# Optimization experiments

Hardware: AMD Instinct MI355X
Metric: run time of the kernel (lower is better)

## Reference

```python
import jax, jax.numpy as jnp
import numpy as np

N_NODES = 50000
N_EDGES = 600000
IN_CH = 64
HID = 128
N_GRAPHS = 64
EPS = 0.0  # GINEConv default eps


def setup_inputs() -> dict:
    key = jax.random.key(0)
    ks = jax.random.split(key, 16)
    x = jax.random.normal(ks[0], (N_NODES, IN_CH), dtype=jnp.float32)
    edge_index = jax.random.randint(ks[1], (2, N_EDGES), 0, N_NODES, dtype=jnp.int64)
    edge_attr = jax.random.normal(ks[2], (N_EDGES, 3), dtype=jnp.float32)
    batch = jnp.sort(jax.random.randint(ks[3], (N_NODES,), 0, N_GRAPHS, dtype=jnp.int64))
    s = lambda fan_in: 1.0 / np.sqrt(fan_in)
    # conv1: edge lin (3->IN_CH), mlp (IN_CH->HID->HID)
    el1_w = jax.random.uniform(ks[4], (3, IN_CH), minval=-s(3), maxval=s(3))
    el1_b = jnp.zeros((IN_CH,), jnp.float32)
    w1a = jax.random.uniform(ks[5], (IN_CH, HID), minval=-s(IN_CH), maxval=s(IN_CH))
    b1a = jnp.zeros((HID,), jnp.float32)
    w1b = jax.random.uniform(ks[6], (HID, HID), minval=-s(HID), maxval=s(HID))
    b1b = jnp.zeros((HID,), jnp.float32)
    # conv2: edge lin (3->HID), mlp (HID->HID->HID)
    el2_w = jax.random.uniform(ks[7], (3, HID), minval=-s(3), maxval=s(3))
    el2_b = jnp.zeros((HID,), jnp.float32)
    w2a = jax.random.uniform(ks[8], (HID, HID), minval=-s(HID), maxval=s(HID))
    b2a = jnp.zeros((HID,), jnp.float32)
    w2b = jax.random.uniform(ks[9], (HID, HID), minval=-s(HID), maxval=s(HID))
    b2b = jnp.zeros((HID,), jnp.float32)
    return dict(x=x, edge_index=edge_index, edge_attr=edge_attr, batch=batch,
                el1_w=el1_w, el1_b=el1_b, w1a=w1a, b1a=b1a, w1b=w1b, b1b=b1b,
                el2_w=el2_w, el2_b=el2_b, w2a=w2a, b2a=b2a, w2b=w2b, b2b=b2b)


def _gine_conv(x, src, dst, edge_attr, el_w, el_b, wa, ba, wb, bb):
    # message: relu(x_j + Lin(edge_attr)), aggregated (sum) at target nodes
    e = edge_attr @ el_w + el_b              # [E, d]
    msg = jax.nn.relu(x[src] + e)            # [E, d]
    agg = jax.ops.segment_sum(msg, dst, num_segments=x.shape[0])  # [N, d]
    h = (1.0 + EPS) * x + agg
    h = jax.nn.relu(h @ wa + ba) @ wb + bb   # MLP
    return h


def reference(x, edge_index, edge_attr, batch,
              el1_w, el1_b, w1a, b1a, w1b, b1b,
              el2_w, el2_b, w2a, b2a, w2b, b2b):
    src, dst = edge_index[0], edge_index[1]
    h = jax.nn.relu(_gine_conv(x, src, dst, edge_attr, el1_w, el1_b, w1a, b1a, w1b, b1b))
    h = jax.nn.relu(_gine_conv(h, src, dst, edge_attr, el2_w, el2_b, w2a, b2a, w2b, b2b))
    # global mean pool per graph
    sums = jax.ops.segment_sum(h, batch, num_segments=N_GRAPHS)
    cnt = jax.ops.segment_sum(jnp.ones((h.shape[0],), h.dtype), batch, num_segments=N_GRAPHS)
    return sums / jnp.maximum(cnt, 1.0)[:, None]
```

## Files before the change

kernel.cpp:

```cpp
#include <hip/hip_runtime.h>

#define N_NODES 50000
#define N_EDGES 600000
#define N_PAD 50048
#define IN_CH 64
#define HID 128
#define N_GRAPHS 64
#define CAP 64
#define CAP_SHIFT 6

typedef __attribute__((ext_vector_type(8))) short bf16x8;
typedef __attribute__((ext_vector_type(4))) float f32x4;

__device__ __forceinline__ float bf2f(unsigned short u) {
    union { unsigned int i; float f; } v; v.i = ((unsigned int)u) << 16; return v.f;
}
__device__ __forceinline__ unsigned short f2bf(float f) {
    union { float f; unsigned int i; } v; v.f = f;
    unsigned int u = v.i;
    return (unsigned short)((u + 0x7FFFu + ((u >> 16) & 1u)) >> 16);
}


__global__ void prep_kernel(const float* __restrict__ x,
                            const float* __restrict__ w1a, const float* __restrict__ w1b,
                            const float* __restrict__ w2a, const float* __restrict__ w2b,
                            const int* __restrict__ batch,
                            unsigned short* __restrict__ xbf,
                            unsigned short* __restrict__ waT1, unsigned short* __restrict__ wbT1,
                            unsigned short* __restrict__ waT2, unsigned short* __restrict__ wbT2,
                            int* __restrict__ deg, float* __restrict__ out,
                            float* __restrict__ inv_cnt) {
    int i = blockIdx.x * blockDim.x + threadIdx.x;
    if (i < N_NODES * IN_CH) xbf[i] = f2bf(x[i]);
    if (i < N_NODES) deg[i] = 0;
    if (i < N_GRAPHS * HID) out[i] = 0.f;
    if (i < N_GRAPHS) {
        int g = i;
        int lo = 0, hi = N_NODES;
        while (lo < hi) { int mid = (lo + hi) >> 1; if (batch[mid] < g) lo = mid + 1; else hi = mid; }
        int start = lo;
        lo = 0; hi = N_NODES;
        while (lo < hi) { int mid = (lo + hi) >> 1; if (batch[mid] <= g) lo = mid + 1; else hi = mid; }
        float c = (float)(lo - start);
        inv_cnt[g] = 1.0f / (c > 1.0f ? c : 1.0f);
    }
    if (i < IN_CH * HID) {
        int k = i / HID, n = i % HID;
        waT1[n * IN_CH + k] = f2bf(w1a[i]);
    }
    if (i < HID * HID) {
        int k = i / HID, n = i % HID;
        wbT1[n * HID + k] = f2bf(w1b[i]);
        waT2[n * HID + k] = f2bf(w2a[i]);
        wbT2[n * HID + k] = f2bf(w2b[i]);
    }
}

__global__ void build_kernel(const int* __restrict__ ei,
                             const float* __restrict__ ea,
                             int* __restrict__ deg,
                             uint2* __restrict__ edata) {
    int i = blockIdx.x * blockDim.x + threadIdx.x;
    if (i >= N_EDGES) return;
    int s = ei[i];
    int d = ei[N_EDGES + i];
    float a0 = ea[3 * (size_t)i], a1 = ea[3 * (size_t)i + 1], a2 = ea[3 * (size_t)i + 2];
    int p = atomicAdd(&deg[d], 1);
    if (p < CAP)
        edata[((size_t)d << CAP_SHIFT) + p] =
            make_uint2((unsigned)s | ((unsigned)f2bf(a0) << 16),
                       (unsigned)f2bf(a1) | ((unsigned)f2bf(a2) << 16));
}

__global__ void gather64_kernel(const unsigned short* __restrict__ xin,
                                const uint2* __restrict__ edata,
                                const int* __restrict__ deg,
                                const float* __restrict__ elw,
                                const float* __restrict__ elb,
                                unsigned short* __restrict__ sg) {
    constexpr int K = IN_CH;
    constexpr int NPB = 4;
    const int node0 = blockIdx.x * NPB;
    const int t = threadIdx.x;
    const int c = t & 63, half = t >> 6;
    const float w0 = elw[c], w1 = elw[K + c], w2 = elw[2 * K + c], eb = elb[c];

    auto term = [&](uint2 e, unsigned short row) -> float {
        float ev = bf2f((unsigned short)(e.x >> 16)) * w0 +
                   bf2f((unsigned short)(e.y & 0xFFFF)) * w1 +
                   bf2f((unsigned short)(e.y >> 16)) * w2 + eb;
        float m = bf2f(row) + ev;
        return m > 0.f ? m : 0.f;
    };

    for (int i = 0; i < NPB; i += 2) {
        int node = node0 + i + half;
        float acc = bf2f(xin[(size_t)node * K + c]);
        int dn = deg[node]; if (dn > CAP) dn = CAP;
        int jb = node << CAP_SHIFT, je = jb + dn;
        int j = jb;
        for (; j + 8 <= je; j += 8) {
            uint2 e0 = edata[j],     e1 = edata[j + 1], e2 = edata[j + 2], e3 = edata[j + 3];
            uint2 e4 = edata[j + 4], e5 = edata[j + 5], e6 = edata[j + 6], e7 = edata[j + 7];
            unsigned short r0 = xin[(size_t)(e0.x & 0xFFFF) * K + c];
            unsigned short r1 = xin[(size_t)(e1.x & 0xFFFF) * K + c];
            unsigned short r2 = xin[(size_t)(e2.x & 0xFFFF) * K + c];
            unsigned short r3 = xin[(size_t)(e3.x & 0xFFFF) * K + c];
            unsigned short r4 = xin[(size_t)(e4.x & 0xFFFF) * K + c];
            unsigned short r5 = xin[(size_t)(e5.x & 0xFFFF) * K + c];
            unsigned short r6 = xin[(size_t)(e6.x & 0xFFFF) * K + c];
            unsigned short r7 = xin[(size_t)(e7.x & 0xFFFF) * K + c];
            acc += term(e0, r0) + term(e1, r1) + term(e2, r2) + term(e3, r3)
                 + term(e4, r4) + term(e5, r5) + term(e6, r6) + term(e7, r7);
        }
        for (; j + 4 <= je; j += 4) {
            uint2 e0 = edata[j], e1 = edata[j + 1], e2 = edata[j + 2], e3 = edata[j + 3];
            unsigned short r0 = xin[(size_t)(e0.x & 0xFFFF) * K + c];
            unsigned short r1 = xin[(size_t)(e1.x & 0xFFFF) * K + c];
            unsigned short r2 = xin[(size_t)(e2.x & 0xFFFF) * K + c];
            unsigned short r3 = xin[(size_t)(e3.x & 0xFFFF) * K + c];
            acc += term(e0, r0) + term(e1, r1) + term(e2, r2) + term(e3, r3);
        }
        for (; j < je; j++) {
            uint2 e0 = edata[j];
            acc += term(e0, xin[(size_t)(e0.x & 0xFFFF) * K + c]);
        }
        sg[(size_t)node * K + c] = f2bf(acc);
    }
}

__global__ void gather128_kernel(const unsigned short* __restrict__ xin,
                                 const uint2* __restrict__ edata,
                                 const int* __restrict__ deg,
                                 const float* __restrict__ elw,
                                 const float* __restrict__ elb,
                                 unsigned short* __restrict__ sg) {
    const int t = threadIdx.x;
    const int w = t >> 6, l = t & 63;
    const unsigned* x32 = (const unsigned*)xin;
    unsigned* sg32 = (unsigned*)sg;
    const int c0 = 2 * l;
    const float w00 = elw[c0],           w01 = elw[c0 + 1];
    const float w10 = elw[HID + c0],     w11 = elw[HID + c0 + 1];
    const float w20 = elw[2 * HID + c0], w21 = elw[2 * HID + c0 + 1];
    const float eb0 = elb[c0],           eb1 = elb[c0 + 1];
    const int nA = (blockIdx.x * 4 + w) * 2;
    const int nB = nA + 1;

    unsigned svA = x32[(size_t)nA * 64 + l];
    unsigned svB = x32[(size_t)nB * 64 + l];
    float a0 = bf2f((unsigned short)(svA & 0xFFFF));
    float a1 = bf2f((unsigned short)(svA >> 16));
    float b0 = bf2f((unsigned short)(svB & 0xFFFF));
    float b1 = bf2f((unsigned short)(svB >> 16));

    auto term2 = [&](uint2 e, unsigned r, float& p0, float& p1) {
        float A0 = bf2f((unsigned short)(e.x >> 16));
        float A1 = bf2f((unsigned short)(e.y & 0xFFFF));
        float A2 = bf2f((unsigned short)(e.y >> 16));
        float ev0 = A0 * w00 + A1 * w10 + A2 * w20 + eb0;
        float ev1 = A0 * w01 + A1 * w11 + A2 * w21 + eb1;
        float m0 = bf2f((unsigned short)(r & 0xFFFF)) + ev0;
        float m1 = bf2f((unsigned short)(r >> 16)) + ev1;
        p0 += m0 > 0.f ? m0 : 0.f;
        p1 += m1 > 0.f ? m1 : 0.f;
    };

    int dA = deg[nA]; if (dA > CAP) dA = CAP;
    int dB = deg[nB]; if (dB > CAP) dB = CAP;
    int ja = nA << CAP_SHIFT; const int jaE = ja + dA;
    int jb = nB << CAP_SHIFT; const int jbE = jb + dB;
    while (ja + 4 <= jaE && jb + 4 <= jbE) {
        uint2 eA0 = edata[ja],     eA1 = edata[ja + 1], eA2 = edata[ja + 2], eA3 = edata[ja + 3];
        uint2 eB0 = edata[jb],     eB1 = edata[jb + 1], eB2 = edata[jb + 2], eB3 = edata[jb + 3];
        unsigned rA0 = x32[(size_t)(eA0.x & 0xFFFF) * 64 + l];
        unsigned rA1 = x32[(size_t)(eA1.x & 0xFFFF) * 64 + l];
        unsigned rA2 = x32[(size_t)(eA2.x & 0xFFFF) * 64 + l];
        unsigned rA3 = x32[(size_t)(eA3.x & 0xFFFF) * 64 + l];
        unsigned rB0 = x32[(size_t)(eB0.x & 0xFFFF) * 64 + l];
        unsigned rB1 = x32[(size_t)(eB1.x & 0xFFFF) * 64 + l];
        unsigned rB2 = x32[(size_t)(eB2.x & 0xFFFF) * 64 + l];
        unsigned rB3 = x32[(size_t)(eB3.x & 0xFFFF) * 64 + l];
        term2(eA0, rA0, a0, a1); term2(eA1, rA1, a0, a1);
        term2(eA2, rA2, a0, a1); term2(eA3, rA3, a0, a1);
        term2(eB0, rB0, b0, b1); term2(eB1, rB1, b0, b1);
        term2(eB2, rB2, b0, b1); term2(eB3, rB3, b0, b1);
        ja += 4; jb += 4;
    }
    for (; ja + 4 <= jaE; ja += 4) {
        uint2 e0 = edata[ja], e1 = edata[ja + 1], e2 = edata[ja + 2], e3 = edata[ja + 3];
        unsigned r0 = x32[(size_t)(e0.x & 0xFFFF) * 64 + l];
        unsigned r1 = x32[(size_t)(e1.x & 0xFFFF) * 64 + l];
        unsigned r2 = x32[(size_t)(e2.x & 0xFFFF) * 64 + l];
        unsigned r3 = x32[(size_t)(e3.x & 0xFFFF) * 64 + l];
        term2(e0, r0, a0, a1); term2(e1, r1, a0, a1);
        term2(e2, r2, a0, a1); term2(e3, r3, a0, a1);
    }
    for (; ja < jaE; ja++) {
        uint2 e0 = edata[ja];
        term2(e0, x32[(size_t)(e0.x & 0xFFFF) * 64 + l], a0, a1);
    }
    for (; jb + 4 <= jbE; jb += 4) {
        uint2 e0 = edata[jb], e1 = edata[jb + 1], e2 = edata[jb + 2], e3 = edata[jb + 3];
        unsigned r0 = x32[(size_t)(e0.x & 0xFFFF) * 64 + l];
        unsigned r1 = x32[(size_t)(e1.x & 0xFFFF) * 64 + l];
        unsigned r2 = x32[(size_t)(e2.x & 0xFFFF) * 64 + l];
        unsigned r3 = x32[(size_t)(e3.x & 0xFFFF) * 64 + l];
        term2(e0, r0, b0, b1); term2(e1, r1, b0, b1);
        term2(e2, r2, b0, b1); term2(e3, r3, b0, b1);
    }
    for (; jb < jbE; jb++) {
        uint2 e0 = edata[jb];
        term2(e0, x32[(size_t)(e0.x & 0xFFFF) * 64 + l], b0, b1);
    }
    sg32[(size_t)nA * 64 + l] = (unsigned)f2bf(a0) | ((unsigned)f2bf(a1) << 16);
    sg32[(size_t)nB * 64 + l] = (unsigned)f2bf(b0) | ((unsigned)f2bf(b1) << 16);
}

template <int K, bool POOL>
__global__ __launch_bounds__(256)
void mlp_mfma_kernel(const unsigned short* __restrict__ sg,
                     const unsigned short* __restrict__ waT,
                     const float* __restrict__ ba,
                     const unsigned short* __restrict__ wbT,
                     const float* __restrict__ bb,
                     void* __restrict__ outv,
                     const int* __restrict__ batch,
                     const float* __restrict__ inv_cnt) {
    constexpr int HSTR = 136;
    constexpr int OSTR = HID + 4;
    __shared__ __align__(16) unsigned short sHid[4][16 * HSTR];
    __shared__ __align__(16) float sOut[64 * OSTR];
    const int t = threadIdx.x;
    const int w = t >> 6, l = t & 63;
    const int i16 = l & 15, q = l >> 4;
    const int blk0 = blockIdx.x * 64;
    const int row0 = blk0 + w * 16;

    bf16x8 aA[K / 32];
    #pragma unroll
    for (int s = 0; s < K / 32; s++)
        aA[s] = *(const bf16x8*)&sg[(size_t)(row0 + i16) * K + s * 32 + q * 8];
    unsigned short* myHid = sHid[w];
    #pragma unroll
    for (int ct = 0; ct < 8; ct++) {
        int col = ct * 16 + i16;
        float bv = ba[col];
        f32x4 acc = (f32x4){bv, bv, bv, bv};
        #pragma unroll
        for (int s = 0; s < K / 32; s++) {
            bf16x8 b = *(const bf16x8*)&waT[(size_t)col * K + s * 32 + q * 8];
            acc = __builtin_amdgcn_mfma_f32_16x16x32_bf16(aA[s], b, acc, 0, 0, 0);
        }
        #pragma unroll
        for (int r = 0; r < 4; r++) {
            float v = acc[r] > 0.f ? acc[r] : 0.f;
            myHid[(q * 4 + r) * HSTR + col] = f2bf(v);
        }
    }
    __syncthreads();

    bf16x8 aB[4];
    #pragma unroll
    for (int s = 0; s < 4; s++)
        aB[s] = *(const bf16x8*)&myHid[i16 * HSTR + s * 32 + q * 8];
    #pragma unroll
    for (int ct = 0; ct < 8; ct++) {
        int col = ct * 16 + i16;
        float bv = bb[col];
        f32x4 acc = (f32x4){bv, bv, bv, bv};
        #pragma unroll
        for (int s = 0; s < 4; s++) {
            bf16x8 b = *(const bf16x8*)&wbT[(size_t)col * HID + s * 32 + q * 8];
            acc = __builtin_amdgcn_mfma_f32_16x16x32_bf16(aB[s], b, acc, 0, 0, 0);
        }
        #pragma unroll
        for (int r = 0; r < 4; r++) {
            float v = acc[r] > 0.f ? acc[r] : 0.f;
            sOut[(w * 16 + q * 4 + r) * OSTR + col] = v;
        }
    }
    __syncthreads();

    if (POOL) {
        if (t < HID) {
            float* out = (float*)outv;
            float acc = 0.f;
            int curg = batch[blk0];
            for (int row = 0; row < 64; row++) {
                int node = blk0 + row;
                if (node >= N_NODES) break;
                int g = batch[node];
                if (g != curg) {
                    atomicAdd(&out[curg * HID + t], acc * inv_cnt[curg]);
                    acc = 0.f; curg = g;
                }
                acc += sOut[row * OSTR + t];
            }
            atomicAdd(&out[curg * HID + t], acc * inv_cnt[curg]);
        }
    } else {
        unsigned short* hout = (unsigned short*)outv;
        for (int idx = t; idx < 64 * 16; idx += 256) {
            int row = idx >> 4, ch = idx & 15;
            int node = blk0 + row;
            if (node < N_NODES) {
                float4 f0 = *(const float4*)&sOut[row * OSTR + ch * 8];
                float4 f1 = *(const float4*)&sOut[row * OSTR + ch * 8 + 4];
                uint4 u;
                u.x = (unsigned)f2bf(f0.x) | ((unsigned)f2bf(f0.y) << 16);
                u.y = (unsigned)f2bf(f0.z) | ((unsigned)f2bf(f0.w) << 16);
                u.z = (unsigned)f2bf(f1.x) | ((unsigned)f2bf(f1.y) << 16);
                u.w = (unsigned)f2bf(f1.z) | ((unsigned)f2bf(f1.w) << 16);
                *(uint4*)&hout[(size_t)node * HID + ch * 8] = u;
            }
        }
    }
}

extern "C" void kernel_launch(void* const* d_in, const int* in_sizes, int n_in,
                              void* d_out, int out_size, void* d_ws, size_t ws_size,
                              hipStream_t stream) {
    const float* x    = (const float*)d_in[0];
    const int*   ei   = (const int*)d_in[1];
    const float* ea   = (const float*)d_in[2];
    const int*   batch= (const int*)d_in[3];
    const float* el1w = (const float*)d_in[4];
    const float* el1b = (const float*)d_in[5];
    const float* w1a  = (const float*)d_in[6];
    const float* b1a  = (const float*)d_in[7];
    const float* w1b  = (const float*)d_in[8];
    const float* b1b  = (const float*)d_in[9];
    const float* el2w = (const float*)d_in[10];
    const float* el2b = (const float*)d_in[11];
    const float* w2a  = (const float*)d_in[12];
    const float* b2a  = (const float*)d_in[13];
    const float* w2b  = (const float*)d_in[14];
    const float* b2b  = (const float*)d_in[15];
    float* out = (float*)d_out;

    uint2* edata    = (uint2*)d_ws;
    float* inv_cnt  = (float*)(edata + (size_t)N_NODES * CAP);
    int*   deg      = (int*)(inv_cnt + N_GRAPHS * HID);
    unsigned short* hbf  = (unsigned short*)((char*)inv_cnt + (size_t)58192 * 4);
    unsigned short* sgbuf= hbf + (size_t)N_NODES * HID;
    unsigned short* waT1 = sgbuf + (size_t)N_PAD * HID;
    unsigned short* wbT1 = waT1 + HID * IN_CH;
    unsigned short* waT2 = wbT1 + HID * HID;
    unsigned short* wbT2 = waT2 + HID * HID;
    unsigned short* xbf  = wbT2 + HID * HID;

    prep_kernel<<<(N_NODES * IN_CH) / 256, 256, 0, stream>>>(
        x, w1a, w1b, w2a, w2b, batch, xbf, waT1, wbT1, waT2, wbT2, deg, out, inv_cnt);
    build_kernel<<<(N_EDGES + 255) / 256, 256, 0, stream>>>(ei, ea, deg, edata);

    gather64_kernel<<<N_NODES / 4, 128, 0, stream>>>(
        xbf, edata, deg, el1w, el1b, sgbuf);
    mlp_mfma_kernel<IN_CH, false><<<N_PAD / 64, 256, 0, stream>>>(
        sgbuf, waT1, b1a, wbT1, b1b, hbf, nullptr, nullptr);

    gather128_kernel<<<N_NODES / 8, 256, 0, stream>>>(
        hbf, edata, deg, el2w, el2b, sgbuf);
    mlp_mfma_kernel<HID, true><<<N_PAD / 64, 256, 0, stream>>>(
        sgbuf, waT2, b2a, wbT2, b2b, out, batch, inv_cnt);
}
```

Before: 262.5 us.

## Split edges across lane groups with vectorized feature loads in gather kernels

Both gather kernels now assign one node per wavefront. Each lane loads 4 bf16 features as a uint2, and lane subgroups handle different edges in parallel: 4 edges per step for the 64-wide gather and 2 for the 128-wide one. Partial sums are combined with xor shuffles, and only one subgroup adds the self term and writes the result. This aims to raise memory-level parallelism and cut per-edge instruction count compared with scalar per-channel loads. The cost is masked padding edges when the degree is not a multiple of the group size, plus the shuffle reduction.

```diff
diff --git a/kernel.cpp b/kernel.cpp
--- a/kernel.cpp
+++ b/kernel.cpp
@@ -73,149 +73,114 @@
                        (unsigned)f2bf(a1) | ((unsigned)f2bf(a2) << 16));
 }
 
-__global__ void gather64_kernel(const unsigned short* __restrict__ xin,
-                                const uint2* __restrict__ edata,
-                                const int* __restrict__ deg,
-                                const float* __restrict__ elw,
-                                const float* __restrict__ elb,
-                                unsigned short* __restrict__ sg) {
-    constexpr int K = IN_CH;
-    constexpr int NPB = 4;
-    const int node0 = blockIdx.x * NPB;
-    const int t = threadIdx.x;
-    const int c = t & 63, half = t >> 6;
-    const float w0 = elw[c], w1 = elw[K + c], w2 = elw[2 * K + c], eb = elb[c];
-
-    auto term = [&](uint2 e, unsigned short row) -> float {
-        float ev = bf2f((unsigned short)(e.x >> 16)) * w0 +
-                   bf2f((unsigned short)(e.y & 0xFFFF)) * w1 +
-                   bf2f((unsigned short)(e.y >> 16)) * w2 + eb;
-        float m = bf2f(row) + ev;
-        return m > 0.f ? m : 0.f;
-    };
-
-    for (int i = 0; i < NPB; i += 2) {
-        int node = node0 + i + half;
-        float acc = bf2f(xin[(size_t)node * K + c]);
-        int dn = deg[node]; if (dn > CAP) dn = CAP;
-        int jb = node << CAP_SHIFT, je = jb + dn;
-        int j = jb;
-        for (; j + 8 <= je; j += 8) {
-            uint2 e0 = edata[j],     e1 = edata[j + 1], e2 = edata[j + 2], e3 = edata[j + 3];
-            uint2 e4 = edata[j + 4], e5 = edata[j + 5], e6 = edata[j + 6], e7 = edata[j + 7];
-            unsigned short r0 = xin[(size_t)(e0.x & 0xFFFF) * K + c];
-            unsigned short r1 = xin[(size_t)(e1.x & 0xFFFF) * K + c];
-            unsigned short r2 = xin[(size_t)(e2.x & 0xFFFF) * K + c];
-            unsigned short r3 = xin[(size_t)(e3.x & 0xFFFF) * K + c];
-            unsigned short r4 = xin[(size_t)(e4.x & 0xFFFF) * K + c];
-            unsigned short r5 = xin[(size_t)(e5.x & 0xFFFF) * K + c];
-            unsigned short r6 = xin[(size_t)(e6.x & 0xFFFF) * K + c];
-            unsigned short r7 = xin[(size_t)(e7.x & 0xFFFF) * K + c];
-            acc += term(e0, r0) + term(e1, r1) + term(e2, r2) + term(e3, r3)
-                 + term(e4, r4) + term(e5, r5) + term(e6, r6) + term(e7, r7);
-        }
-        for (; j + 4 <= je; j += 4) {
-            uint2 e0 = edata[j], e1 = edata[j + 1], e2 = edata[j + 2], e3 = edata[j + 3];
-            unsigned short r0 = xin[(size_t)(e0.x & 0xFFFF) * K + c];
-            unsigned short r1 = xin[(size_t)(e1.x & 0xFFFF) * K + c];
-            unsigned short r2 = xin[(size_t)(e2.x & 0xFFFF) * K + c];
-            unsigned short r3 = xin[(size_t)(e3.x & 0xFFFF) * K + c];
-            acc += term(e0, r0) + term(e1, r1) + term(e2, r2) + term(e3, r3);
-        }
-        for (; j < je; j++) {
-            uint2 e0 = edata[j];
-            acc += term(e0, xin[(size_t)(e0.x & 0xFFFF) * K + c]);
-        }
-        sg[(size_t)node * K + c] = f2bf(acc);
-    }
-}
-
-__global__ void gather128_kernel(const unsigned short* __restrict__ xin,
-                                 const uint2* __restrict__ edata,
-                                 const int* __restrict__ deg,
-                                 const float* __restrict__ elw,
-                                 const float* __restrict__ elb,
-                                 unsigned short* __restrict__ sg) {
+__global__ __launch_bounds__(256)
+void gather64_kernel(const unsigned short* __restrict__ xin,
+                     const uint2* __restrict__ edata,
+                     const int* __restrict__ deg,
+                     const float* __restrict__ elw,
+                     const float* __restrict__ elb,
+                     unsigned short* __restrict__ sg) {
     const int t = threadIdx.x;
     const int w = t >> 6, l = t & 63;
-    const unsigned* x32 = (const unsigned*)xin;
-    unsigned* sg32 = (unsigned*)sg;
-    const int c0 = 2 * l;
-    const float w00 = elw[c0],           w01 = elw[c0 + 1];
-    const float w10 = elw[HID + c0],     w11 = elw[HID + c0 + 1];
-    const float w20 = elw[2 * HID + c0], w21 = elw[2 * HID + c0 + 1];
-    const float eb0 = elb[c0],           eb1 = elb[c0 + 1];
-    const int nA = (blockIdx.x * 4 + w) * 2;
-    const int nB = nA + 1;
-
-    unsigned svA = x32[(size_t)nA * 64 + l];
-    unsigned svB = x32[(size_t)nB * 64 + l];
-    float a0 = bf2f((unsigned short)(svA & 0xFFFF));
-    float a1 = bf2f((unsigned short)(svA >> 16));
-    float b0 = bf2f((unsigned short)(svB & 0xFFFF));
-    float b1 = bf2f((unsigned short)(svB >> 16));
-
-    auto term2 = [&](uint2 e, unsigned r, float& p0, float& p1) {
+    const int s = l >> 4;
+    const int c = 4 * (l & 15);
+    const int node = blockIdx.x * 4 + w;
+
+    const float4 w0 = *(const float4*)&elw[c];
+    const float4 w1 = *(const float4*)&elw[64 + c];
+    const float4 w2 = *(const float4*)&elw[128 + c];
+    const float4 eb = *(const float4*)&elb[c];
+
+    float a0 = 0.f, a1 = 0.f, a2 = 0.f, a3 = 0.f;
+    int dn = deg[node]; if (dn > CAP) dn = CAP;
+    const int base = node << CAP_SHIFT;
+    for (int j0 = 0; j0 < dn; j0 += 4) {
+        uint2 e = edata[base + j0 + s];
+        bool valid = (j0 + s) < dn;
+        unsigned src = valid ? (e.x & 0xFFFFu) : 0u;
         float A0 = bf2f((unsigned short)(e.x >> 16));
         float A1 = bf2f((unsigned short)(e.y & 0xFFFF));
         float A2 = bf2f((unsigned short)(e.y >> 16));
-        float ev0 = A0 * w00 + A1 * w10 + A2 * w20 + eb0;
-        float ev1 = A0 * w01 + A1 * w11 + A2 * w21 + eb1;
-        float m0 = bf2f((unsigned short)(r & 0xFFFF)) + ev0;
-        float m1 = bf2f((unsigned short)(r >> 16)) + ev1;
-        p0 += m0 > 0.f ? m0 : 0.f;
-        p1 += m1 > 0.f ? m1 : 0.f;
-    };
-
-    int dA = deg[nA]; if (dA > CAP) dA = CAP;
-    int dB = deg[nB]; if (dB > CAP) dB = CAP;
-    int ja = nA << CAP_SHIFT; const int jaE = ja + dA;
-    int jb = nB << CAP_SHIFT; const int jbE = jb + dB;
-    while (ja + 4 <= jaE && jb + 4 <= jbE) {
-        uint2 eA0 = edata[ja],     eA1 = edata[ja + 1], eA2 = edata[ja + 2], eA3 = edata[ja + 3];
-        uint2 eB0 = edata[jb],     eB1 = edata[jb + 1], eB2 = edata[jb + 2], eB3 = edata[jb + 3];
-        unsigned rA0 = x32[(size_t)(eA0.x & 0xFFFF) * 64 + l];
-        unsigned rA1 = x32[(size_t)(eA1.x & 0xFFFF) * 64 + l];
-        unsigned rA2 = x32[(size_t)(eA2.x & 0xFFFF) * 64 + l];
-        unsigned rA3 = x32[(size_t)(eA3.x & 0xFFFF) * 64 + l];
-        unsigned rB0 = x32[(size_t)(eB0.x & 0xFFFF) * 64 + l];
-        unsigned rB1 = x32[(size_t)(eB1.x & 0xFFFF) * 64 + l];
-        unsigned rB2 = x32[(size_t)(eB2.x & 0xFFFF) * 64 + l];
-        unsigned rB3 = x32[(size_t)(eB3.x & 0xFFFF) * 64 + l];
-        term2(eA0, rA0, a0, a1); term2(eA1, rA1, a0, a1);
-        term2(eA2, rA2, a0, a1); term2(eA3, rA3, a0, a1);
-        term2(eB0, rB0, b0, b1); term2(eB1, rB1, b0, b1);
-        term2(eB2, rB2, b0, b1); term2(eB3, rB3, b0, b1);
-        ja += 4; jb += 4;
-    }
-    for (; ja + 4 <= jaE; ja += 4) {
-        uint2 e0 = edata[ja], e1 = edata[ja + 1], e2 = edata[ja + 2], e3 = edata[ja + 3];
-        unsigned r0 = x32[(size_t)(e0.x & 0xFFFF) * 64 + l];
-        unsigned r1 = x32[(size_t)(e1.x & 0xFFFF) * 64 + l];
-        unsigned r2 = x32[(size_t)(e2.x & 0xFFFF) * 64 + l];
-        unsigned r3 = x32[(size_t)(e3.x & 0xFFFF) * 64 + l];
-        term2(e0, r0, a0, a1); term2(e1, r1, a0, a1);
-        term2(e2, r2, a0, a1); term2(e3, r3, a0, a1);
-    }
-    for (; ja < jaE; ja++) {
-        uint2 e0 = edata[ja];
-        term2(e0, x32[(size_t)(e0.x & 0xFFFF) * 64 + l], a0, a1);
-    }
-    for (; jb + 4 <= jbE; jb += 4) {
-        uint2 e0 = edata[jb], e1 = edata[jb + 1], e2 = edata[jb + 2], e3 = edata[jb + 3];
-        unsigned r0 = x32[(size_t)(e0.x & 0xFFFF) * 64 + l];
-        unsigned r1 = x32[(size_t)(e1.x & 0xFFFF) * 64 + l];
-        unsigned r2 = x32[(size_t)(e2.x & 0xFFFF) * 64 + l];
-        unsigned r3 = x32[(size_t)(e3.x & 0xFFFF) * 64 + l];
-        term2(e0, r0, b0, b1); term2(e1, r1, b0, b1);
-        term2(e2, r2, b0, b1); term2(e3, r3, b0, b1);
-    }
-    for (; jb < jbE; jb++) {
-        uint2 e0 = edata[jb];
-        term2(e0, x32[(size_t)(e0.x & 0xFFFF) * 64 + l], b0, b1);
-    }
-    sg32[(size_t)nA * 64 + l] = (unsigned)f2bf(a0) | ((unsigned)f2bf(a1) << 16);
-    sg32[(size_t)nB * 64 + l] = (unsigned)f2bf(b0) | ((unsigned)f2bf(b1) << 16);
+        uint2 r = *(const uint2*)&xin[(size_t)src * 64 + c];
+        float m0 = bf2f((unsigned short)(r.x & 0xFFFF)) + A0 * w0.x + A1 * w1.x + A2 * w2.x + eb.x;
+        float m1 = bf2f((unsigned short)(r.x >> 16))    + A0 * w0.y + A1 * w1.y + A2 * w2.y + eb.y;
+        float m2 = bf2f((unsigned short)(r.y & 0xFFFF)) + A0 * w0.z + A1 * w1.z + A2 * w2.z + eb.z;
+        float m3 = bf2f((unsigned short)(r.y >> 16))    + A0 * w0.w + A1 * w1.w + A2 * w2.w + eb.w;
+        m0 = m0 > 0.f ? m0 : 0.f;  m1 = m1 > 0.f ? m1 : 0.f;
+        m2 = m2 > 0.f ? m2 : 0.f;  m3 = m3 > 0.f ? m3 : 0.f;
+        a0 += valid ? m0 : 0.f;  a1 += valid ? m1 : 0.f;
+        a2 += valid ? m2 : 0.f;  a3 += valid ? m3 : 0.f;
+    }
+    a0 += __shfl_xor(a0, 16); a0 += __shfl_xor(a0, 32);
+    a1 += __shfl_xor(a1, 16); a1 += __shfl_xor(a1, 32);
+    a2 += __shfl_xor(a2, 16); a2 += __shfl_xor(a2, 32);
+    a3 += __shfl_xor(a3, 16); a3 += __shfl_xor(a3, 32);
+    if (s == 0) {
+        uint2 sv = *(const uint2*)&xin[(size_t)node * 64 + c];
+        a0 += bf2f((unsigned short)(sv.x & 0xFFFF));
+        a1 += bf2f((unsigned short)(sv.x >> 16));
+        a2 += bf2f((unsigned short)(sv.y & 0xFFFF));
+        a3 += bf2f((unsigned short)(sv.y >> 16));
+        uint2 o;
+        o.x = (unsigned)f2bf(a0) | ((unsigned)f2bf(a1) << 16);
+        o.y = (unsigned)f2bf(a2) | ((unsigned)f2bf(a3) << 16);
+        *(uint2*)&sg[(size_t)node * 64 + c] = o;
+    }
+}
+
+__global__ __launch_bounds__(256)
+void gather128_kernel(const unsigned short* __restrict__ xin,
+                      const uint2* __restrict__ edata,
+                      const int* __restrict__ deg,
+                      const float* __restrict__ elw,
+                      const float* __restrict__ elb,
+                      unsigned short* __restrict__ sg) {
+    const int t = threadIdx.x;
+    const int w = t >> 6, l = t & 63;
+    const int s = l >> 5;
+    const int c = 4 * (l & 31);
+    const int node = blockIdx.x * 4 + w;
+
+    const float4 w0 = *(const float4*)&elw[c];
+    const float4 w1 = *(const float4*)&elw[HID + c];
+    const float4 w2 = *(const float4*)&elw[2 * HID + c];
+    const float4 eb = *(const float4*)&elb[c];
+
+    float a0 = 0.f, a1 = 0.f, a2 = 0.f, a3 = 0.f;
+    int dn = deg[node]; if (dn > CAP) dn = CAP;
+    const int base = node << CAP_SHIFT;
+    for (int j0 = 0; j0 < dn; j0 += 2) {
+        uint2 e = edata[base + j0 + s];
+        bool valid = (j0 + s) < dn;
+        unsigned src = valid ? (e.x & 0xFFFFu) : 0u;
+        float A0 = bf2f((unsigned short)(e.x >> 16));
+        float A1 = bf2f((unsigned short)(e.y & 0xFFFF));
+        float A2 = bf2f((unsigned short)(e.y >> 16));
+        uint2 r = *(const uint2*)&xin[(size_t)src * 128 + c];
+        float m0 = bf2f((unsigned short)(r.x & 0xFFFF)) + A0 * w0.x + A1 * w1.x + A2 * w2.x + eb.x;
+        float m1 = bf2f((unsigned short)(r.x >> 16))    + A0 * w0.y + A1 * w1.y + A2 * w2.y + eb.y;
+        float m2 = bf2f((unsigned short)(r.y & 0xFFFF)) + A0 * w0.z + A1 * w1.z + A2 * w2.z + eb.z;
+        float m3 = bf2f((unsigned short)(r.y >> 16))    + A0 * w0.w + A1 * w1.w + A2 * w2.w + eb.w;
+        m0 = m0 > 0.f ? m0 : 0.f;  m1 = m1 > 0.f ? m1 : 0.f;
+        m2 = m2 > 0.f ? m2 : 0.f;  m3 = m3 > 0.f ? m3 : 0.f;
+        a0 += valid ? m0 : 0.f;  a1 += valid ? m1 : 0.f;
+        a2 += valid ? m2 : 0.f;  a3 += valid ? m3 : 0.f;
+    }
+    a0 += __shfl_xor(a0, 32);
+    a1 += __shfl_xor(a1, 32);
+    a2 += __shfl_xor(a2, 32);
+    a3 += __shfl_xor(a3, 32);
+    if (s == 0) {
+        uint2 sv = *(const uint2*)&xin[(size_t)node * 128 + c];
+        a0 += bf2f((unsigned short)(sv.x & 0xFFFF));
+        a1 += bf2f((unsigned short)(sv.x >> 16));
+        a2 += bf2f((unsigned short)(sv.y & 0xFFFF));
+        a3 += bf2f((unsigned short)(sv.y >> 16));
+        uint2 o;
+        o.x = (unsigned)f2bf(a0) | ((unsigned)f2bf(a1) << 16);
+        o.y = (unsigned)f2bf(a2) | ((unsigned)f2bf(a3) << 16);
+        *(uint2*)&sg[(size_t)node * 128 + c] = o;
+    }
 }
 
 template <int K, bool POOL>
@@ -355,12 +320,12 @@
         x, w1a, w1b, w2a, w2b, batch, xbf, waT1, wbT1, waT2, wbT2, deg, out, inv_cnt);
     build_kernel<<<(N_EDGES + 255) / 256, 256, 0, stream>>>(ei, ea, deg, edata);
 
-    gather64_kernel<<<N_NODES / 4, 128, 0, stream>>>(
+    gather64_kernel<<<N_NODES / 4, 256, 0, stream>>>(
         xbf, edata, deg, el1w, el1b, sgbuf);
     mlp_mfma_kernel<IN_CH, false><<<N_PAD / 64, 256, 0, stream>>>(
         sgbuf, waT1, b1a, wbT1, b1b, hbf, nullptr, nullptr);
 
-    gather128_kernel<<<N_NODES / 8, 256, 0, stream>>>(
+    gather128_kernel<<<N_NODES / 4, 256, 0, stream>>>(
         hbf, edata, deg, el2w, el2b, sgbuf);
     mlp_mfma_kernel<HID, true><<<N_PAD / 64, 256, 0, stream>>>(
         sgbuf, waT2, b2a, wbT2, b2b, out, batch, inv_cnt);
```

Measured after the change: 280.5 us. +6.9%, slower.
